# Kernel tuning notes

Measured on AMD Instinct MI355X. Metric: run time of the kernel, lower is better.

Reference implementation:

```python
import jax, jax.numpy as jnp
import numpy as np

IMAGE_SIZE = (224, 224)
SIGMA = 4.0
KS = 2 * int(4.0 * SIGMA + 0.5) + 1  # 33


def _gaussian_kernel2d(ks, sigma):
    x = jnp.arange(ks, dtype=jnp.float32) - (ks - 1) / 2.0
    g = jnp.exp(-(x ** 2) / (2.0 * sigma ** 2))
    g = g / g.sum()
    return jnp.outer(g, g)  # already sums to 1; normalize_kernel2d is a no-op


def setup_inputs() -> dict:
    key = jax.random.key(0)
    k1, k2, k3 = jax.random.split(key, 3)
    B, C, H, W = 32, 200, 56, 56
    HW = H * W
    embedding = jax.random.normal(k1, (B, C, H, W), dtype=jnp.float32)
    mean = jax.random.normal(k2, (C, HW), dtype=jnp.float32)
    A = jax.random.normal(k3, (HW, C, C), dtype=jnp.float32)
    # PSD per-pixel inverse covariance, as produced by real PaDiM statistics
    inv_covariance = jnp.einsum('nij,nkj->nik', A, A) / C + 0.1 * jnp.eye(C, dtype=jnp.float32)
    covariance = jnp.zeros((1,), dtype=jnp.float32)  # unused on mahalanobis path
    return {"embedding": embedding, "mean": mean,
            "inv_covariance": inv_covariance, "covariance": covariance}


def reference(embedding, mean, inv_covariance, covariance):
    B, C, H, W = embedding.shape
    HW = H * W
    emb = embedding.reshape(B, C, HW)
    # delta: [HW, B, C]
    delta = jnp.transpose(emb - mean[None], (2, 0, 1))
    # per-pixel mahalanobis quadratic form: diag(delta @ inv_cov @ delta^T)
    md = jnp.matmul(delta, inv_covariance)          # [HW, B, C]
    q = jnp.sum(md * delta, axis=-1)                # [HW, B]
    dist = jnp.sqrt(jnp.clip(q, 0.0, None))
    score = jnp.transpose(dist, (1, 0)).reshape(B, 1, H, W)
    # bilinear upsample (align_corners=False == half-pixel centers)
    up = jax.image.resize(score, (B, 1, IMAGE_SIZE[0], IMAGE_SIZE[1]), method='bilinear')
    # gaussian blur, reflect 'same' padding, single channel
    kernel = _gaussian_kernel2d(KS, SIGMA)[None, None]  # [1,1,KS,KS]
    pad = (KS - 1) // 2
    padded = jnp.pad(up, ((0, 0), (0, 0), (pad, pad), (pad, pad)), mode='reflect')
    out = jax.lax.conv_general_dilated(padded, kernel, window_strides=(1, 1),
                                       padding='VALID')
    return out
```

## Files before the change

kernel.cpp:

```cpp
#include <hip/hip_runtime.h>
#include <math.h>

#define HW   3136
#define NC   200
#define NB   32
#define SS   56
#define OS   224
#define KS   33
#define GPAD 16

typedef __attribute__((ext_vector_type(8))) short          short8;
typedef __attribute__((ext_vector_type(4))) float          f32x4;
typedef __attribute__((ext_vector_type(4))) unsigned short ush4;

__device__ __forceinline__ unsigned short f2bf(float x) {
    unsigned int u = __builtin_bit_cast(unsigned int, x);
    u += 0x7FFFu + ((u >> 16) & 1u);
    return (unsigned short)(u >> 16);
}
__device__ __forceinline__ float bf2f(unsigned short h) {
    unsigned int u = ((unsigned int)h) << 16;
    return __builtin_bit_cast(float, u);
}

__device__ __forceinline__ void gload16(const void* g, void* l) {
    __builtin_amdgcn_global_load_lds(
        (const __attribute__((address_space(1))) void*)g,
        (__attribute__((address_space(3))) void*)l, 16, 0, 0);
}

__global__ __launch_bounds__(256)
void k_delta(const float* __restrict__ emb,
             const float* __restrict__ mean,
             unsigned short* __restrict__ dg) {
    const int tile = blockIdx.x >> 2;
    const int bq   = blockIdx.x & 3;
    const int n0   = tile * 16;
    const int t    = threadIdx.x;

    __shared__ float          mm[32 * 20];
    __shared__ unsigned short tr[256 * 20];

    unsigned int* dgU = (unsigned int*)dg;

    for (int kt = 0; kt < 7; kt++) {
        const int c0 = kt * 32;
        if (t < 128) {
            int cl = t >> 2, nl4 = (t & 3) * 4;
            int c = c0 + cl;
            float4 v = {0.f, 0.f, 0.f, 0.f};
            if (c < NC) v = *(const float4*)&mean[(size_t)c * HW + n0 + nl4];
            *(float4*)&mm[cl * 20 + nl4] = v;
        }
        __syncthreads();
#pragma unroll
        for (int j = 0; j < 4; j++) {
            int row = (t >> 2) + 64 * j;
            int nl4 = (t & 3) * 4;
            int b   = bq * 8 + (row >> 5);
            int cl  = row & 31;
            int c   = c0 + cl;
            ush4 wv = {0, 0, 0, 0};
            if (c < NC) {
                float4 e = *(const float4*)&emb[((size_t)(b * NC + c)) * HW + n0 + nl4];
                float4 m = *(const float4*)&mm[cl * 20 + nl4];
                wv[0] = f2bf(e.x - m.x); wv[1] = f2bf(e.y - m.y);
                wv[2] = f2bf(e.z - m.z); wv[3] = f2bf(e.w - m.w);
            }
            *(ush4*)&tr[row * 20 + nl4] = wv;
        }
        __syncthreads();
#pragma unroll
        for (int j = 0; j < 8; j++) {
            int idx = t + 256 * j;
            int nl  = idx >> 7, rem = idx & 127;
            int bl  = rem >> 4, cu = rem & 15;
            int cb  = bl * 32 + 2 * cu;
            unsigned int lo = tr[cb * 20 + nl];
            unsigned int hi = tr[(cb + 1) * 20 + nl];
            dgU[((size_t)(n0 + nl) * 7 + kt) * 512 +
                (size_t)(bq * 8 + bl) * 16 + cu] = lo | (hi << 16);
        }
        __syncthreads();
    }
}

__global__ __launch_bounds__(256, 4)
void k_mahal2(const unsigned short* __restrict__ dg,
              const float* __restrict__ icov,
              float* __restrict__ score) {
    const int bid = blockIdx.x;
    const int n = (bid & 7) * 392 + (bid >> 3);
    const int t = threadIdx.x;

    __shared__ unsigned short dd[7 * 1024];
    __shared__ float slab[2][16 * NC];
    __shared__ float qs[NB];

    const float* Mn   = icov + (size_t)n * (NC * NC);
    const char*  dsrc = (const char*)(dg + (size_t)n * 7168);

    {
        char* lb = (char*)dd;
#pragma unroll
        for (int i = 0; i < 4; i++) {
            int idx = i * 256 + t;
            if (idx < 896)
                gload16(dsrc + (size_t)idx * 16, lb + (i * 256 + (t & 192)) * 16);
        }
        const char* ms = (const char*)Mn;
        char* sb = (char*)&slab[0][0];
#pragma unroll
        for (int i = 0; i < 4; i++) {
            int idx = i * 256 + t;
            if (idx < 800)
                gload16(ms + (size_t)idx * 16, sb + (i * 256 + (t & 192)) * 16);
        }
    }
    if (t < NB) qs[t] = 0.f;
    __syncthreads();

    const int lane = t & 63;
    const int w    = t >> 6;
    const int col  = lane & 15;
    const int quad = lane >> 4;
    const int bt   = w & 1;
    const int kg   = w >> 1;
    const int nk   = kg ? 3 : 4;
    const int ddb  = (bt * 16 + col) * 32;

    short8 bF[4];
#pragma unroll
    for (int q = 0; q < 4; q++) {
        if (q < nk) {
            int kt = kg + 2 * q;
            bF[q] = *(const short8*)&dd[kt * 1024 + ddb + quad * 8];
        }
    }

    const int abase = col * NC + quad * 8;
    float qacc = 0.f;

    for (int it = 0; it < 13; it++) {
        if (it < 12) {
            const int nf4 = (it == 11) ? 400 : 800;
            const char* ms = (const char*)(Mn + (size_t)(it + 1) * 16 * NC);
            char* sb = (char*)&slab[(it + 1) & 1][0];
#pragma unroll
            for (int i = 0; i < 4; i++) {
                int idx = i * 256 + t;
                if (idx < nf4)
                    gload16(ms + (size_t)idx * 16, sb + (i * 256 + (t & 192)) * 16);
            }
        }
        const float* sl = &slab[it & 1][0];
        f32x4 acc = {0.f, 0.f, 0.f, 0.f};
#pragma unroll
        for (int q = 0; q < 4; q++) {
            if (q < nk) {
                int kt = kg + 2 * q;
                const f32x4* ap = (const f32x4*)&sl[abase + kt * 32];
                f32x4 lo = ap[0], hi = ap[1];
                short8 aF;
                aF[0] = f2bf(lo[0]); aF[1] = f2bf(lo[1]);
                aF[2] = f2bf(lo[2]); aF[3] = f2bf(lo[3]);
                aF[4] = f2bf(hi[0]); aF[5] = f2bf(hi[1]);
                aF[6] = f2bf(hi[2]); aF[7] = f2bf(hi[3]);
                acc = __builtin_amdgcn_mfma_f32_16x16x32_bf16(aF, bF[q], acc, 0, 0, 0);
            }
        }
        {
            int off = (it >> 1) * 1024 + ddb + (it & 1) * 16 + quad * 4;
            ush4 dv = *(const ush4*)&dd[off];
            float v = acc[0] * bf2f(dv[0]) + acc[1] * bf2f(dv[1]) +
                      acc[2] * bf2f(dv[2]) + acc[3] * bf2f(dv[3]);
            v += __shfl_xor(v, 16);
            v += __shfl_xor(v, 32);
            qacc += v;
        }
        __syncthreads();
    }

    if (quad == 0) atomicAdd(&qs[bt * 16 + col], qacc);
    __syncthreads();
    if (t < NB) {
        float q = qs[t];
        score[(size_t)t * HW + n] = sqrtf(q > 0.f ? q : 0.f);
    }
}

__global__ void k_upsample(const float* __restrict__ score,
                           float* __restrict__ up) {
    int idx = blockIdx.x * 256 + threadIdx.x;
    if (idx >= NB * OS * OS) return;
    int x = idx % OS;
    int y = (idx / OS) % OS;
    int b = idx / (OS * OS);

    float sy = 0.25f * y - 0.375f;
    float sx = 0.25f * x - 0.375f;
    int y0 = (int)floorf(sy); float fy = sy - (float)y0;
    int x0 = (int)floorf(sx); float fx = sx - (float)x0;
    int y0c = min(max(y0, 0), SS - 1), y1c = min(max(y0 + 1, 0), SS - 1);
    int x0c = min(max(x0, 0), SS - 1), x1c = min(max(x0 + 1, 0), SS - 1);

    const float* sb = score + (size_t)b * HW;
    float v00 = sb[y0c * SS + x0c];
    float v01 = sb[y0c * SS + x1c];
    float v10 = sb[y1c * SS + x0c];
    float v11 = sb[y1c * SS + x1c];
    up[idx] = (1.f - fy) * ((1.f - fx) * v00 + fx * v01) +
              fy * ((1.f - fx) * v10 + fx * v11);
}

__global__ void k_gauss_init(float* __restrict__ g) {
    if (threadIdx.x == 0) {
        float e[KS];
        float sum = 0.f;
        for (int i = 0; i < KS; i++) {
            float x = (float)i - 16.0f;
            e[i] = expf(-(x * x) / 32.0f);
            sum += e[i];
        }
        for (int i = 0; i < KS; i++) g[i] = e[i] / sum;
    }
}

__device__ __forceinline__ int reflect224(int i) {
    if (i < 0) return -i;
    if (i > OS - 1) return 2 * (OS - 1) - i;
    return i;
}

__global__ void k_hblur(const float* __restrict__ up,
                        const float* __restrict__ g,
                        float* __restrict__ tmp) {
    int idx = blockIdx.x * 256 + threadIdx.x;
    if (idx >= NB * OS * OS) return;
    int x = idx % OS;
    int row = idx / OS;
    const float* src = up + (size_t)row * OS;
    float acc = 0.f;
#pragma unroll
    for (int t = -GPAD; t <= GPAD; t++) {
        acc += g[t + GPAD] * src[reflect224(x + t)];
    }
    tmp[idx] = acc;
}

__global__ void k_vblur(const float* __restrict__ tmp,
                        const float* __restrict__ g,
                        float* __restrict__ out) {
    int idx = blockIdx.x * 256 + threadIdx.x;
    if (idx >= NB * OS * OS) return;
    int x = idx % OS;
    int y = (idx / OS) % OS;
    int b = idx / (OS * OS);
    const float* src = tmp + (size_t)b * OS * OS;
    float acc = 0.f;
#pragma unroll
    for (int t = -GPAD; t <= GPAD; t++) {
        acc += g[t + GPAD] * src[(size_t)reflect224(y + t) * OS + x];
    }
    out[idx] = acc;
}

extern "C" void kernel_launch(void* const* d_in, const int* in_sizes, int n_in,
                              void* d_out, int out_size, void* d_ws, size_t ws_size,
                              hipStream_t stream) {
    const float* emb  = (const float*)d_in[0];
    const float* mean = (const float*)d_in[1];
    const float* icov = (const float*)d_in[2];
    float* out = (float*)d_out;

    char* ws = (char*)d_ws;
    float* g     = (float*)ws;
    float* score = (float*)(ws + 256);
    float* tmp   = (float*)(ws + 256 + 401408);
    unsigned short* dg = (unsigned short*)(ws + 6824192);

    const int up_blocks = (NB * OS * OS) / 256;

    k_gauss_init<<<1, 64, 0, stream>>>(g);
    k_delta<<<784, 256, 0, stream>>>(emb, mean, dg);
    k_mahal2<<<HW, 256, 0, stream>>>(dg, icov, score);
    k_upsample<<<up_blocks, 256, 0, stream>>>(score, out);
    k_hblur<<<up_blocks, 256, 0, stream>>>(out, g, tmp);
    k_vblur<<<up_blocks, 256, 0, stream>>>(tmp, g, out);
}
```

Measured before the change: 752.4 us.

## Exploit inverse-covariance symmetry to load and multiply only the lower triangle

Because the per-pixel inverse covariance is symmetric, the quadratic form can use only the lower-triangular blocks: off-diagonal 16-wide blocks are weighted by 2 and diagonal blocks by 1. Each slab iteration now fetches only the columns up to the current row block into a padded-stride shared layout, and skips MFMA tiles entirely above the diagonal. This roughly halves the global traffic on the dominant icov read, at the cost of more index arithmetic and a loop that now has to be fully unrolled.

```diff
diff --git a/kernel.cpp b/kernel.cpp
--- a/kernel.cpp
+++ b/kernel.cpp
@@ -93,8 +93,8 @@
     const int n = (bid & 7) * 392 + (bid >> 3);
     const int t = threadIdx.x;
 
-    __shared__ unsigned short dd[7 * 1024];
-    __shared__ float slab[2][16 * NC];
+    __shared__ __align__(16) unsigned short dd[7 * 1024];
+    __shared__ __align__(16) float slab[2][3200];
     __shared__ float qs[NB];
 
     const float* Mn   = icov + (size_t)n * (NC * NC);
@@ -110,11 +110,13 @@
         }
         const char* ms = (const char*)Mn;
         char* sb = (char*)&slab[0][0];
-#pragma unroll
-        for (int i = 0; i < 4; i++) {
-            int idx = i * 256 + t;
-            if (idx < 800)
-                gload16(ms + (size_t)idx * 16, sb + (i * 256 + (t & 192)) * 16);
+        if (t < 88) {
+            int row = t / 5;
+            int c   = t - row * 5;
+            if (row >= 16) { row = 15; c = 0; }
+            if (c >= 4) c = 0;
+            gload16(ms + (size_t)row * (NC * 4) + (size_t)c * 16,
+                    sb + (t & 192) * 16);
         }
     }
     if (t < NB) qs[t] = 0.f;
@@ -126,50 +128,71 @@
     const int quad = lane >> 4;
     const int bt   = w & 1;
     const int kg   = w >> 1;
-    const int nk   = kg ? 3 : 4;
     const int ddb  = (bt * 16 + col) * 32;
 
     short8 bF[4];
 #pragma unroll
     for (int q = 0; q < 4; q++) {
-        if (q < nk) {
-            int kt = kg + 2 * q;
+        int kt = kg + 2 * q;
+        if (kt < 7)
             bF[q] = *(const short8*)&dd[kt * 1024 + ddb + quad * 8];
-        }
-    }
-
-    const int abase = col * NC + quad * 8;
+    }
+
     float qacc = 0.f;
 
+#pragma unroll
     for (int it = 0; it < 13; it++) {
         if (it < 12) {
-            const int nf4 = (it == 11) ? 400 : 800;
-            const char* ms = (const char*)(Mn + (size_t)(it + 1) * 16 * NC);
-            char* sb = (char*)&slab[(it + 1) & 1][0];
+            const int tt  = it + 1;
+            const int nr  = (tt == 12) ? 8 : 16;
+            const int CHn = (4 * (tt + 1) < 50) ? 4 * (tt + 1) : 50;
+            const int CHpn = CHn + 1;
+            const int T   = nr * CHpn + 8;
+            const char* ms = (const char*)(Mn + (size_t)tt * 16 * NC);
+            char* sb = (char*)&slab[tt & 1][0];
 #pragma unroll
             for (int i = 0; i < 4; i++) {
                 int idx = i * 256 + t;
-                if (idx < nf4)
-                    gload16(ms + (size_t)idx * 16, sb + (i * 256 + (t & 192)) * 16);
+                if (idx < T) {
+                    int row = idx / CHpn;
+                    int c   = idx - row * CHpn;
+                    if (row >= nr) { row = nr - 1; c = 0; }
+                    if (c >= CHn) c = 0;
+                    gload16(ms + (size_t)row * (NC * 4) + (size_t)c * 16,
+                            sb + (i * 256 + (t & 192)) * 16);
+                }
             }
         }
-        const float* sl = &slab[it & 1][0];
-        f32x4 acc = {0.f, 0.f, 0.f, 0.f};
-#pragma unroll
-        for (int q = 0; q < 4; q++) {
-            if (q < nk) {
-                int kt = kg + 2 * q;
-                const f32x4* ap = (const f32x4*)&sl[abase + kt * 32];
-                f32x4 lo = ap[0], hi = ap[1];
-                short8 aF;
-                aF[0] = f2bf(lo[0]); aF[1] = f2bf(lo[1]);
-                aF[2] = f2bf(lo[2]); aF[3] = f2bf(lo[3]);
-                aF[4] = f2bf(hi[0]); aF[5] = f2bf(hi[1]);
-                aF[6] = f2bf(hi[2]); aF[7] = f2bf(hi[3]);
-                acc = __builtin_amdgcn_mfma_f32_16x16x32_bf16(aF, bF[q], acc, 0, 0, 0);
+        {
+            const int CH   = (4 * (it + 1) < 50) ? 4 * (it + 1) : 50;
+            const int strd = (CH + 1) * 4;
+            const int Cq   = (it + 2) >> 1;
+            const int ig   = 16 * it + col;
+            const float* sl = &slab[it & 1][0];
+            f32x4 acc = {0.f, 0.f, 0.f, 0.f};
+#pragma unroll
+            for (int q = 0; q < 4; q++) {
+                const int cq = kg + 2 * q;
+                if (cq < Cq) {
+                    const int half0 = 32 * cq + (quad >> 1) * 16;
+                    float s = 0.f;
+                    if (ig < NC) {
+                        if (half0 + 16 <= 16 * it) s = 2.f;
+                        else if (half0 == 16 * it) s = 1.f;
+                    }
+                    short8 aF = {0, 0, 0, 0, 0, 0, 0, 0};
+                    if (s != 0.f) {
+                        const f32x4* ap =
+                            (const f32x4*)&sl[col * strd + cq * 32 + quad * 8];
+                        f32x4 lo = ap[0], hi = ap[1];
+                        aF[0] = f2bf(s * lo[0]); aF[1] = f2bf(s * lo[1]);
+                        aF[2] = f2bf(s * lo[2]); aF[3] = f2bf(s * lo[3]);
+                        aF[4] = f2bf(s * hi[0]); aF[5] = f2bf(s * hi[1]);
+                        aF[6] = f2bf(s * hi[2]); aF[7] = f2bf(s * hi[3]);
+                    }
+                    acc = __builtin_amdgcn_mfma_f32_16x16x32_bf16(aF, bF[q], acc, 0, 0, 0);
+                }
             }
-        }
-        {
             int off = (it >> 1) * 1024 + ddb + (it & 1) * 16 + quad * 4;
             ush4 dv = *(const ush4*)&dd[off];
             float v = acc[0] * bf2f(dv[0]) + acc[1] * bf2f(dv[1]) +
```

Measured after the change: 720.1 us. 4.3% less time.
